# Performance work log

Hardware: AMD Instinct MI355X
Metric: run time of the kernel (lower is better)

The kernel has to match this reference:

```python
import jax, jax.numpy as jnp
import numpy as np

N = 8192
H = 512
E = 262144
NUM_LAYERS = 2
LAYER_DECAY = 0.4
INIT_W = 1e-05


def setup_inputs() -> dict:
    key = jax.random.key(0)
    ks = jax.random.split(key, 6)
    x = jax.random.normal(ks[0], (N, H), dtype=jnp.float32)
    rows = jax.random.randint(ks[1], (E,), 0, N, dtype=jnp.int32)
    cols = jax.random.randint(ks[2], (E,), 0, N, dtype=jnp.int32)
    vals = jax.random.uniform(ks[3], (E,), dtype=jnp.float32)
    # near-identity init as in GSS_GNNLayer (torch Linear: y = x @ W.T + b)
    W1 = jax.random.normal(ks[4], (H, H), dtype=jnp.float32) * INIT_W + jnp.eye(H, dtype=jnp.float32)
    b1 = jnp.zeros((H,), dtype=jnp.float32)
    W2 = jax.random.normal(ks[5], (H, H), dtype=jnp.float32) * INIT_W + jnp.eye(H, dtype=jnp.float32)
    b2 = jnp.zeros((H,), dtype=jnp.float32)
    return {"x": x, "rows": rows, "cols": cols, "vals": vals,
            "W1": W1, "b1": b1, "W2": W2, "b2": b2}


def _spmm(rows, cols, vals, dense):
    # sparse [N,N] @ dense [N,H] via gather + segment-sum scatter-add
    return jax.ops.segment_sum(vals[:, None] * dense[cols], rows, num_segments=N)


def _gcn_layer(x, rows, cols, vals, W1, b1, W2, b2):
    Ax = _spmm(rows, cols, vals, x)                      # [N,H]
    pre1 = Ax @ W1.T + b1
    Ax_x = _spmm(rows, cols, vals, Ax * x)               # A(Ax * x)
    pre2 = Ax_x @ W2.T + b2
    pre = pre1 + pre2
    return pre, jax.nn.elu(pre)


def reference(x, rows, cols, vals, W1, b1, W2, b2):
    residual = None
    for _ in range(NUM_LAYERS):  # shared weights across layers, as in source
        pre, x = _gcn_layer(x, rows, cols, vals, W1, b1, W2, b2)
        if residual is not None:
            x = residual + LAYER_DECAY * x
        residual = pre
    # decoder: row-wise L2 normalize (eps=1e-12 like F.normalize), dense gram, relu
    norm = jnp.maximum(jnp.linalg.norm(x, axis=1, keepdims=True), 1e-12)
    hidden_emb = x / norm
    adj_preds = jax.nn.relu(hidden_emb @ hidden_emb.T)   # [N,N]
    return adj_preds, hidden_emb
```

## Files before the change

kernel.cpp:

```cpp
#include <hip/hip_runtime.h>

#define N_NODES 8192
#define HDIM    512
#define NEDGE   262144

typedef __attribute__((ext_vector_type(8))) short bf16x8;
typedef __attribute__((ext_vector_type(4))) float f32x4;

__device__ inline unsigned short f2bf(float f) {
  unsigned u = __float_as_uint(f);
  unsigned r = (u + 0x7FFFu + ((u >> 16) & 1u)) >> 16;
  return (unsigned short)r;
}
__device__ inline float bf2f(short s) {
  return __uint_as_float(((unsigned)(unsigned short)s) << 16);
}

__device__ inline void gload16(const void* g, void* l) {
  __builtin_amdgcn_global_load_lds(
      (const __attribute__((address_space(1))) unsigned*)g,
      (__attribute__((address_space(3))) unsigned*)l, 16, 0, 0);
}

__device__ inline void wait_vmcnt_c(int n) {
  if (n == 8)      asm volatile("s_waitcnt vmcnt(8)" ::: "memory");
  else if (n == 4) asm volatile("s_waitcnt vmcnt(4)" ::: "memory");
  else if (n == 3) asm volatile("s_waitcnt vmcnt(3)" ::: "memory");
  else             asm volatile("s_waitcnt vmcnt(0)" ::: "memory");
}

__global__ __launch_bounds__(1024) void scan_kernel(const int* __restrict__ counts,
                                                    int* __restrict__ offs,
                                                    int* __restrict__ cursor) {
  __shared__ int s[1024];
  int tid = threadIdx.x;
  int local[8];
  int sum = 0;
#pragma unroll
  for (int i = 0; i < 8; ++i) { local[i] = counts[tid * 8 + i]; sum += local[i]; }
  s[tid] = sum;
  __syncthreads();
  for (int d = 1; d < 1024; d <<= 1) {
    int v = (tid >= d) ? s[tid - d] : 0;
    __syncthreads();
    s[tid] += v;
    __syncthreads();
  }
  int base = (tid > 0) ? s[tid - 1] : 0;
#pragma unroll
  for (int i = 0; i < 8; ++i) {
    offs[tid * 8 + i] = base;
    cursor[tid * 8 + i] = base;
    base += local[i];
  }
  if (tid == 1023) offs[8192] = base;
}

__global__ void scatter_kernel(const int* __restrict__ rows, const int* __restrict__ cols,
                               const float* __restrict__ vals, int* cursor,
                               int2* __restrict__ edges) {
  int e = blockIdx.x * 256 + threadIdx.x;
  int slot = atomicAdd(&cursor[rows[e]], 1);
  edges[slot] = make_int2(cols[e], __float_as_int(vals[e]));
}

template <int MODE>
__global__ __launch_bounds__(256) void spmm_bf(const int* __restrict__ offs,
                                               const int2* __restrict__ edges,
                                               const short* __restrict__ Xbf,
                                               const float* __restrict__ aux,
                                               short* __restrict__ outb,
                                               short* __restrict__ prodb) {
  int row = blockIdx.x * 4 + (threadIdx.x >> 6);
  int lane = threadIdx.x & 63;
  int h0 = lane * 8;
  float acc[8] = {0.f, 0.f, 0.f, 0.f, 0.f, 0.f, 0.f, 0.f};
  int e0 = offs[row], e1 = offs[row + 1];
  int p = e0;

  int2 ma0, ma1, ma2, ma3;
  bf16x8 xa0, xa1, xa2, xa3;

  if (p + 4 <= e1) {
    ma0 = edges[p]; ma1 = edges[p + 1]; ma2 = edges[p + 2]; ma3 = edges[p + 3];
    xa0 = *reinterpret_cast<const bf16x8*>(Xbf + (size_t)ma0.x * HDIM + h0);
    xa1 = *reinterpret_cast<const bf16x8*>(Xbf + (size_t)ma1.x * HDIM + h0);
    xa2 = *reinterpret_cast<const bf16x8*>(Xbf + (size_t)ma2.x * HDIM + h0);
    xa3 = *reinterpret_cast<const bf16x8*>(Xbf + (size_t)ma3.x * HDIM + h0);
    p += 4;
    for (; p + 4 <= e1; p += 4) {
      int2 mb0 = edges[p], mb1 = edges[p + 1], mb2 = edges[p + 2], mb3 = edges[p + 3];
      bf16x8 xb0 = *reinterpret_cast<const bf16x8*>(Xbf + (size_t)mb0.x * HDIM + h0);
      bf16x8 xb1 = *reinterpret_cast<const bf16x8*>(Xbf + (size_t)mb1.x * HDIM + h0);
      bf16x8 xb2 = *reinterpret_cast<const bf16x8*>(Xbf + (size_t)mb2.x * HDIM + h0);
      bf16x8 xb3 = *reinterpret_cast<const bf16x8*>(Xbf + (size_t)mb3.x * HDIM + h0);
      float v0 = __int_as_float(ma0.y), v1 = __int_as_float(ma1.y);
      float v2 = __int_as_float(ma2.y), v3 = __int_as_float(ma3.y);
#pragma unroll
      for (int j = 0; j < 8; ++j) {
        acc[j] = fmaf(v0, bf2f(xa0[j]), acc[j]);
        acc[j] = fmaf(v1, bf2f(xa1[j]), acc[j]);
        acc[j] = fmaf(v2, bf2f(xa2[j]), acc[j]);
        acc[j] = fmaf(v3, bf2f(xa3[j]), acc[j]);
      }
      ma0 = mb0; ma1 = mb1; ma2 = mb2; ma3 = mb3;
      xa0 = xb0; xa1 = xb1; xa2 = xb2; xa3 = xb3;
    }
    {
      float v0 = __int_as_float(ma0.y), v1 = __int_as_float(ma1.y);
      float v2 = __int_as_float(ma2.y), v3 = __int_as_float(ma3.y);
#pragma unroll
      for (int j = 0; j < 8; ++j) {
        acc[j] = fmaf(v0, bf2f(xa0[j]), acc[j]);
        acc[j] = fmaf(v1, bf2f(xa1[j]), acc[j]);
        acc[j] = fmaf(v2, bf2f(xa2[j]), acc[j]);
        acc[j] = fmaf(v3, bf2f(xa3[j]), acc[j]);
      }
    }
  }
  for (; p < e1; ++p) {
    int2 e = edges[p];
    float v = __int_as_float(e.y);
    bf16x8 xr = *reinterpret_cast<const bf16x8*>(Xbf + (size_t)e.x * HDIM + h0);
#pragma unroll
    for (int j = 0; j < 8; ++j) acc[j] = fmaf(v, bf2f(xr[j]), acc[j]);
  }

  bf16x8 o;
#pragma unroll
  for (int j = 0; j < 8; ++j) o[j] = (short)f2bf(acc[j]);
  *reinterpret_cast<bf16x8*>(outb + (size_t)row * 1024 + h0) = o;
  if (MODE != 2) {
    const float4* ap = reinterpret_cast<const float4*>(aux + (size_t)row * HDIM + h0);
    float4 a0 = ap[0], a1 = ap[1];
    float xv[8] = {a0.x, a0.y, a0.z, a0.w, a1.x, a1.y, a1.z, a1.w};
    if (MODE == 1) {
#pragma unroll
      for (int j = 0; j < 8; ++j) xv[j] = xv[j] > 0.f ? xv[j] : expm1f(xv[j]);
    }
    bf16x8 t;
#pragma unroll
    for (int j = 0; j < 8; ++j) t[j] = (short)f2bf(acc[j] * xv[j]);
    *reinterpret_cast<bf16x8*>(prodb + (size_t)row * HDIM + h0) = t;
  }
}

__device__ inline void cast8(const float* src, short* dst) {
  const float4* p = reinterpret_cast<const float4*>(src);
  float4 a = p[0], b = p[1];
  bf16x8 o;
  o[0] = (short)f2bf(a.x); o[1] = (short)f2bf(a.y);
  o[2] = (short)f2bf(a.z); o[3] = (short)f2bf(a.w);
  o[4] = (short)f2bf(b.x); o[5] = (short)f2bf(b.y);
  o[6] = (short)f2bf(b.z); o[7] = (short)f2bf(b.w);
  *reinterpret_cast<bf16x8*>(dst) = o;
}

__global__ void prep_kernel(const int* __restrict__ rows, int* __restrict__ counts,
                            const float* __restrict__ x,
                            const float* __restrict__ W1, const float* __restrict__ W2,
                            const float* __restrict__ b1, const float* __restrict__ b2,
                            short* __restrict__ Xbf, short* __restrict__ Bbuf,
                            float* __restrict__ b12) {
  int b = blockIdx.x;
  if (b < 1024) {
    int e = b * 256 + threadIdx.x;
    atomicAdd(&counts[rows[e]], 1);
  } else if (b < 3072) {
    int t = (b - 1024) * 256 + threadIdx.x;
    int row = t >> 6, c0 = (t & 63) * 8;
    cast8(x + (size_t)row * 512 + c0, Xbf + (size_t)row * 512 + c0);
  } else if (b < 3200) {
    int t = (b - 3072) * 256 + threadIdx.x;
    int row = t >> 6, c0 = (t & 63) * 8;
    cast8(W1 + (size_t)row * 512 + c0, Bbuf + (size_t)row * 1024 + c0);
  } else if (b < 3328) {
    int t = (b - 3200) * 256 + threadIdx.x;
    int row = t >> 6, c0 = (t & 63) * 8;
    cast8(W2 + (size_t)row * 512 + c0, Bbuf + (size_t)row * 1024 + 512 + c0);
  } else {
    int j = threadIdx.x;
    b12[j] = b1[j] + b2[j];
    b12[j + 256] = b1[j + 256] + b2[j + 256];
  }
}

__global__ __launch_bounds__(256) void rownorm_kernel(const float* __restrict__ X,
                                                      float* __restrict__ outf,
                                                      short* __restrict__ outb) {
  int row = blockIdx.x * 4 + (threadIdx.x >> 6);
  int lane = threadIdx.x & 63;
  int h0 = lane * 8;
  const float4* p = reinterpret_cast<const float4*>(X + (size_t)row * HDIM + h0);
  float4 a = p[0], b = p[1];
  float s = a.x * a.x + a.y * a.y + a.z * a.z + a.w * a.w +
            b.x * b.x + b.y * b.y + b.z * b.z + b.w * b.w;
#pragma unroll
  for (int off = 1; off < 64; off <<= 1) s += __shfl_xor(s, off, 64);
  float inv = 1.f / fmaxf(sqrtf(s), 1e-12f);
  a.x *= inv; a.y *= inv; a.z *= inv; a.w *= inv;
  b.x *= inv; b.y *= inv; b.z *= inv; b.w *= inv;
  float4* q = reinterpret_cast<float4*>(outf + (size_t)row * HDIM + h0);
  q[0] = a; q[1] = b;
  bf16x8 o;
  o[0] = (short)f2bf(a.x); o[1] = (short)f2bf(a.y);
  o[2] = (short)f2bf(a.z); o[3] = (short)f2bf(a.w);
  o[4] = (short)f2bf(b.x); o[5] = (short)f2bf(b.y);
  o[6] = (short)f2bf(b.z); o[7] = (short)f2bf(b.w);
  *reinterpret_cast<bf16x8*>(outb + (size_t)row * HDIM + h0) = o;
}

template <int MODE>
__global__ __launch_bounds__(256) void gemm_ring(const short* __restrict__ A,
                                                 const short* __restrict__ B,
                                                 int N, int K, int nbn,
                                                 const float* __restrict__ bias,
                                                 const float* __restrict__ resid,
                                                 float* __restrict__ out0,
                                                 short* __restrict__ out1bf) {
  __shared__ __align__(16) char lds[3 * 16384];
  int NK = K >> 5;

  int q = gridDim.x >> 3;
  int id = (blockIdx.x & 7) * q + (blockIdx.x >> 3);
  int bn = (id % nbn) * 128;
  int bm = (id / nbn) * 128;

  int tid = threadIdx.x;
  int wid = tid >> 6;
  int lane = tid & 63;
  int wm = wid >> 1, wn = wid & 1;
  int rlo = lane & 15;
  int khi = lane >> 4;
  int wbase = wid * 1024;

  size_t ldkB = (size_t)K * 2;
  const char* Ab = (const char*)A + (size_t)bm * ldkB;
  const char* Bb = (const char*)B + (size_t)bn * ldkB;
  int r4 = tid >> 2, c4 = tid & 3;

  f32x4 zero = {0.f, 0.f, 0.f, 0.f};
  f32x4 acc[4][4];
#pragma unroll
  for (int m = 0; m < 4; ++m)
#pragma unroll
    for (int n = 0; n < 4; ++n) acc[m][n] = zero;

  auto stage = [&](int s) {
    char* slot = lds + (s % 3) * 16384;
    size_t go = (size_t)s * 64 + c4 * 16;
    gload16(Ab + (size_t)r4 * ldkB + go,         slot + wbase);
    gload16(Ab + (size_t)(r4 + 64) * ldkB + go,  slot + 4096 + wbase);
    gload16(Bb + (size_t)r4 * ldkB + go,         slot + 8192 + wbase);
    gload16(Bb + (size_t)(r4 + 64) * ldkB + go,  slot + 12288 + wbase);
  };

  stage(0);
  stage(1);

  for (int s = 0; s < NK; ++s) {
    wait_vmcnt_c((s + 1 < NK) ? 4 : 0);
    __builtin_amdgcn_s_barrier();
    __builtin_amdgcn_sched_barrier(0);
    if (s + 2 < NK) stage(s + 2);

    const char* slot = lds + (s % 3) * 16384;
    bf16x8 av[4], bv[4];
#pragma unroll
    for (int m = 0; m < 4; ++m)
      av[m] = *reinterpret_cast<const bf16x8*>(
          slot + (wm * 64 + m * 16 + rlo) * 64 + khi * 16);
#pragma unroll
    for (int n = 0; n < 4; ++n)
      bv[n] = *reinterpret_cast<const bf16x8*>(
          slot + 8192 + (wn * 64 + n * 16 + rlo) * 64 + khi * 16);

    __builtin_amdgcn_s_setprio(1);
#pragma unroll
    for (int m = 0; m < 4; ++m)
#pragma unroll
      for (int n = 0; n < 4; ++n)
        acc[m][n] = __builtin_amdgcn_mfma_f32_16x16x32_bf16(av[m], bv[n], acc[m][n], 0, 0, 0);
    __builtin_amdgcn_s_setprio(0);
  }

  int obm = bm + wm * 64;
  int obn = bn + wn * 64;
  int crow = khi * 4;
#pragma unroll
  for (int n = 0; n < 4; ++n) {
    int c = obn + n * 16 + rlo;
    float bc = bias[c];
#pragma unroll
    for (int m = 0; m < 4; ++m) {
#pragma unroll
      for (int v = 0; v < 4; ++v) {
        int r = obm + m * 16 + crow + v;
        size_t idx = (size_t)r * N + c;
        float val = acc[m][n][v];
        if (MODE == 0) {
          float pvl = val + bc;
          out0[idx] = pvl;
          float e = pvl > 0.f ? pvl : expm1f(pvl);
          out1bf[idx] = (short)f2bf(e);
        } else {
          float pvl = val + bc;
          out0[idx] = resid[idx] + 0.4f * (pvl > 0.f ? pvl : expm1f(pvl));
        }
      }
    }
  }
}

__global__ __launch_bounds__(512, 4) void gram256(const short* __restrict__ H,
                                                  float* __restrict__ out) {
  __shared__ __align__(16) char lds[3 * 24576];
  const int NK = HDIM / 32;

  int id = (blockIdx.x & 7) * 256 + (blockIdx.x >> 3);
  int st = id >> 4, wt = id & 15;
  int bm = ((st >> 3) * 4 + (wt >> 2)) * 128;
  int bn = ((st & 7) * 4 + (wt & 3)) * 256;

  int tid = threadIdx.x;
  int wid = tid >> 6;
  int lane = tid & 63;
  int wr = wid >> 2;
  int wc = wid & 3;
  int rlo = lane & 15;
  int khi = lane >> 4;
  int wbase = wid * 1024;

  const char* Ab = (const char*)H + (size_t)bm * 1024;
  const char* Bb = (const char*)H + (size_t)bn * 1024;
  int r4 = tid >> 2, c4 = tid & 3;

  f32x4 zero = {0.f, 0.f, 0.f, 0.f};
  f32x4 acc[4][4];
#pragma unroll
  for (int m = 0; m < 4; ++m)
#pragma unroll
    for (int n = 0; n < 4; ++n) acc[m][n] = zero;

  auto stage = [&](int s) {
    char* slot = lds + (s % 3) * 24576;
    size_t go = (size_t)s * 64 + c4 * 16;
    gload16(Ab + (size_t)r4 * 1024 + go,         slot + wbase);
    gload16(Bb + (size_t)r4 * 1024 + go,         slot + 8192 + wbase);
    gload16(Bb + (size_t)(r4 + 128) * 1024 + go, slot + 16384 + wbase);
  };

  stage(0);
  stage(1);

  for (int s = 0; s < NK; ++s) {
    wait_vmcnt_c((s + 1 < NK) ? 3 : 0);
    __builtin_amdgcn_s_barrier();
    __builtin_amdgcn_sched_barrier(0);
    if (s + 2 < NK) stage(s + 2);

    const char* slot = lds + (s % 3) * 24576;
    bf16x8 av[4], bv[4];
#pragma unroll
    for (int m = 0; m < 4; ++m)
      av[m] = *reinterpret_cast<const bf16x8*>(
          slot + (wr * 64 + m * 16 + rlo) * 64 + khi * 16);
#pragma unroll
    for (int n = 0; n < 4; ++n)
      bv[n] = *reinterpret_cast<const bf16x8*>(
          slot + 8192 + (wc * 64 + n * 16 + rlo) * 64 + khi * 16);

    __builtin_amdgcn_s_setprio(1);
#pragma unroll
    for (int m = 0; m < 4; ++m)
#pragma unroll
      for (int n = 0; n < 4; ++n)
        acc[m][n] = __builtin_amdgcn_mfma_f32_16x16x32_bf16(av[m], bv[n], acc[m][n], 0, 0, 0);
    __builtin_amdgcn_s_setprio(0);
  }

  int obm = bm + wr * 64;
  int obn = bn + wc * 64;
  int crow = khi * 4;
#pragma unroll
  for (int m = 0; m < 4; ++m) {
#pragma unroll
    for (int n = 0; n < 4; ++n) {
      int c = obn + n * 16 + rlo;
#pragma unroll
      for (int v = 0; v < 4; ++v) {
        int r = obm + m * 16 + crow + v;
        float val = acc[m][n][v];
        out[(size_t)r * N_NODES + c] = val > 0.f ? val : 0.f;
      }
    }
  }
}

extern "C" void kernel_launch(void* const* d_in, const int* in_sizes, int n_in,
                              void* d_out, int out_size, void* d_ws, size_t ws_size,
                              hipStream_t stream) {
  const float* x  = (const float*)d_in[0];
  const int* rows = (const int*)d_in[1];
  const int* cols = (const int*)d_in[2];
  const float* vals = (const float*)d_in[3];
  const float* W1 = (const float*)d_in[4];
  const float* b1 = (const float*)d_in[5];
  const float* W2 = (const float*)d_in[6];
  const float* b2 = (const float*)d_in[7];

  float* out_adj = (float*)d_out;
  float* out_hid = out_adj + (size_t)N_NODES * N_NODES;

  char* w = (char*)d_ws;
  size_t off = 0;
  auto alloc = [&](size_t bytes) -> void* {
    void* p = w + off;
    off += (bytes + 255) & ~(size_t)255;
    return p;
  };
  int* counts   = (int*)alloc(8192 * sizeof(int));
  int* offs     = (int*)alloc(8193 * sizeof(int));
  int* cursor   = (int*)alloc(8192 * sizeof(int));
  int2* edges   = (int2*)alloc((size_t)NEDGE * sizeof(int2));
  float* b12    = (float*)alloc(HDIM * sizeof(float));
  short* Xbf    = (short*)alloc((size_t)N_NODES * HDIM * sizeof(short));
  short* Tbf    = (short*)alloc((size_t)N_NODES * HDIM * sizeof(short));
  short* Abuf   = (short*)alloc((size_t)N_NODES * 1024 * sizeof(short));
  short* Bbuf   = (short*)alloc((size_t)512 * 1024 * sizeof(short));
  float* pre1   = (float*)alloc((size_t)N_NODES * HDIM * sizeof(float));
  float* Hf     = (float*)alloc((size_t)N_NODES * HDIM * sizeof(float));
  short* Hbuf   = (short*)alloc((size_t)N_NODES * HDIM * sizeof(short));

  hipMemsetAsync(counts, 0, 8192 * sizeof(int), stream);
  prep_kernel<<<3329, 256, 0, stream>>>(rows, counts, x, W1, W2, b1, b2, Xbf, Bbuf, b12);
  scan_kernel<<<1, 1024, 0, stream>>>(counts, offs, cursor);
  scatter_kernel<<<NEDGE / 256, 256, 0, stream>>>(rows, cols, vals, cursor, edges);

  spmm_bf<0><<<2048, 256, 0, stream>>>(offs, edges, Xbf, x, Abuf, Tbf);
  spmm_bf<2><<<2048, 256, 0, stream>>>(offs, edges, Tbf, nullptr, Abuf + 512, nullptr);
  gemm_ring<0><<<256, 256, 0, stream>>>(Abuf, Bbuf, 512, 1024, 4, b12, nullptr, pre1, Xbf);

  spmm_bf<1><<<2048, 256, 0, stream>>>(offs, edges, Xbf, pre1, Abuf, Tbf);
  spmm_bf<2><<<2048, 256, 0, stream>>>(offs, edges, Tbf, nullptr, Abuf + 512, nullptr);
  gemm_ring<1><<<256, 256, 0, stream>>>(Abuf, Bbuf, 512, 1024, 4, b12, pre1, Hf, nullptr);

  rownorm_kernel<<<2048, 256, 0, stream>>>(Hf, out_hid, Hbuf);
  gram256<<<2048, 512, 0, stream>>>(Hbuf, out_adj);
}
```

Measured before the change: 315.7 us.

## Enlarge gram tile to 256x256 with 8-wave split-phase double-buffered pipeline

Replaces the 128x256 gram kernel with a 256x256 tile per block, so each wave computes a 128x64 output using 8x4 accumulators. The K loop now moves 128 elements per iteration, split into four quarter-loads across two double-buffered 64 KB LDS slots, with loads interleaved between MFMA phases. This halves the number of blocks and raises reuse of the operands fetched from global memory. In exchange it uses more registers, allows fewer resident blocks per CU, and needs a hand-scheduled waitcnt sequence. The gram kernel's output write of the 8192x8192 fp32 matrix is unchanged and probably dominates its cost.

```diff
diff --git a/kernel.cpp b/kernel.cpp
--- a/kernel.cpp
+++ b/kernel.cpp
@@ -24,6 +24,7 @@
 
 __device__ inline void wait_vmcnt_c(int n) {
   if (n == 8)      asm volatile("s_waitcnt vmcnt(8)" ::: "memory");
+  else if (n == 6) asm volatile("s_waitcnt vmcnt(6)" ::: "memory");
   else if (n == 4) asm volatile("s_waitcnt vmcnt(4)" ::: "memory");
   else if (n == 3) asm volatile("s_waitcnt vmcnt(3)" ::: "memory");
   else             asm volatile("s_waitcnt vmcnt(0)" ::: "memory");
@@ -312,14 +313,13 @@
   }
 }
 
-__global__ __launch_bounds__(512, 4) void gram256(const short* __restrict__ H,
-                                                  float* __restrict__ out) {
-  __shared__ __align__(16) char lds[3 * 24576];
-  const int NK = HDIM / 32;
-
-  int id = (blockIdx.x & 7) * 256 + (blockIdx.x >> 3);
+__global__ __launch_bounds__(512, 2) void gram8(const short* __restrict__ H,
+                                                float* __restrict__ out) {
+  __shared__ __align__(16) char lds[131072];
+
+  int id = (blockIdx.x & 7) * 128 + (blockIdx.x >> 3);
   int st = id >> 4, wt = id & 15;
-  int bm = ((st >> 3) * 4 + (wt >> 2)) * 128;
+  int bm = ((st >> 3) * 4 + (wt >> 2)) * 256;
   int bn = ((st & 7) * 4 + (wt & 3)) * 256;
 
   int tid = threadIdx.x;
@@ -336,54 +336,141 @@
   int r4 = tid >> 2, c4 = tid & 3;
 
   f32x4 zero = {0.f, 0.f, 0.f, 0.f};
-  f32x4 acc[4][4];
-#pragma unroll
-  for (int m = 0; m < 4; ++m)
+  f32x4 acc[8][4];
+#pragma unroll
+  for (int m = 0; m < 8; ++m)
 #pragma unroll
     for (int n = 0; n < 4; ++n) acc[m][n] = zero;
 
-  auto stage = [&](int s) {
-    char* slot = lds + (s % 3) * 24576;
-    size_t go = (size_t)s * 64 + c4 * 16;
-    gload16(Ab + (size_t)r4 * 1024 + go,         slot + wbase);
-    gload16(Bb + (size_t)r4 * 1024 + go,         slot + 8192 + wbase);
-    gload16(Bb + (size_t)(r4 + 128) * 1024 + go, slot + 16384 + wbase);
+  auto stage = [&](int kt, int p) {
+    char* buf = lds + ((kt & 1) << 16);
+    int off = (p == 0) ? 0 : (p == 1) ? 32768 : (p == 2) ? 16384 : 49152;
+    const char* src = (p == 0 || p == 2) ? Ab : Bb;
+    size_t go = (size_t)kt * 128 + ((p >> 1) ? 64 : 0) + c4 * 16;
+    gload16(src + (size_t)r4 * 1024 + go,         buf + off + wbase);
+    gload16(src + (size_t)(r4 + 128) * 1024 + go, buf + off + 8192 + wbase);
   };
 
-  stage(0);
-  stage(1);
-
-  for (int s = 0; s < NK; ++s) {
-    wait_vmcnt_c((s + 1 < NK) ? 3 : 0);
+  stage(0, 0); stage(0, 1); stage(0, 2); stage(0, 3);
+
+  bf16x8 av[4], bv[4];
+  const int arow = wr * 128 + rlo;
+  const int brow = wc * 64 + rlo;
+
+#pragma unroll 1
+  for (int kt = 0; kt < 7; ++kt) {
+    const char* buf = lds + ((kt & 1) << 16);
+    stage(kt + 1, 0);
+    wait_vmcnt_c(6);
     __builtin_amdgcn_s_barrier();
     __builtin_amdgcn_sched_barrier(0);
-    if (s + 2 < NK) stage(s + 2);
-
-    const char* slot = lds + (s % 3) * 24576;
-    bf16x8 av[4], bv[4];
-#pragma unroll
-    for (int m = 0; m < 4; ++m)
-      av[m] = *reinterpret_cast<const bf16x8*>(
-          slot + (wr * 64 + m * 16 + rlo) * 64 + khi * 16);
 #pragma unroll
     for (int n = 0; n < 4; ++n)
-      bv[n] = *reinterpret_cast<const bf16x8*>(
-          slot + 8192 + (wc * 64 + n * 16 + rlo) * 64 + khi * 16);
-
+      bv[n] = *reinterpret_cast<const bf16x8*>(buf + 32768 + (brow + n * 16) * 64 + khi * 16);
+#pragma unroll
+    for (int i = 0; i < 4; ++i)
+      av[i] = *reinterpret_cast<const bf16x8*>(buf + (arow + i * 16) * 64 + khi * 16);
     __builtin_amdgcn_s_setprio(1);
 #pragma unroll
-    for (int m = 0; m < 4; ++m)
-#pragma unroll
-      for (int n = 0; n < 4; ++n)
-        acc[m][n] = __builtin_amdgcn_mfma_f32_16x16x32_bf16(av[m], bv[n], acc[m][n], 0, 0, 0);
+    for (int i = 0; i < 4; ++i)
+#pragma unroll
+      for (int n = 0; n < 4; ++n)
+        acc[i][n] = __builtin_amdgcn_mfma_f32_16x16x32_bf16(av[i], bv[n], acc[i][n], 0, 0, 0);
     __builtin_amdgcn_s_setprio(0);
-  }
-
-  int obm = bm + wr * 64;
+    stage(kt + 1, 1);
+#pragma unroll
+    for (int i = 0; i < 4; ++i)
+      av[i] = *reinterpret_cast<const bf16x8*>(buf + (arow + 64 + i * 16) * 64 + khi * 16);
+    __builtin_amdgcn_s_setprio(1);
+#pragma unroll
+    for (int i = 0; i < 4; ++i)
+#pragma unroll
+      for (int n = 0; n < 4; ++n)
+        acc[4 + i][n] = __builtin_amdgcn_mfma_f32_16x16x32_bf16(av[i], bv[n], acc[4 + i][n], 0, 0, 0);
+    __builtin_amdgcn_s_setprio(0);
+    stage(kt + 1, 2);
+    wait_vmcnt_c(6);
+    __builtin_amdgcn_s_barrier();
+    __builtin_amdgcn_sched_barrier(0);
+#pragma unroll
+    for (int n = 0; n < 4; ++n)
+      bv[n] = *reinterpret_cast<const bf16x8*>(buf + 49152 + (brow + n * 16) * 64 + khi * 16);
+#pragma unroll
+    for (int i = 0; i < 4; ++i)
+      av[i] = *reinterpret_cast<const bf16x8*>(buf + 16384 + (arow + i * 16) * 64 + khi * 16);
+    __builtin_amdgcn_s_setprio(1);
+#pragma unroll
+    for (int i = 0; i < 4; ++i)
+#pragma unroll
+      for (int n = 0; n < 4; ++n)
+        acc[i][n] = __builtin_amdgcn_mfma_f32_16x16x32_bf16(av[i], bv[n], acc[i][n], 0, 0, 0);
+    __builtin_amdgcn_s_setprio(0);
+    stage(kt + 1, 3);
+#pragma unroll
+    for (int i = 0; i < 4; ++i)
+      av[i] = *reinterpret_cast<const bf16x8*>(buf + 16384 + (arow + 64 + i * 16) * 64 + khi * 16);
+    __builtin_amdgcn_s_setprio(1);
+#pragma unroll
+    for (int i = 0; i < 4; ++i)
+#pragma unroll
+      for (int n = 0; n < 4; ++n)
+        acc[4 + i][n] = __builtin_amdgcn_mfma_f32_16x16x32_bf16(av[i], bv[n], acc[4 + i][n], 0, 0, 0);
+    __builtin_amdgcn_s_setprio(0);
+  }
+
+  {
+    const char* buf = lds + ((7 & 1) << 16);
+    wait_vmcnt_c(4);
+    __builtin_amdgcn_s_barrier();
+    __builtin_amdgcn_sched_barrier(0);
+#pragma unroll
+    for (int n = 0; n < 4; ++n)
+      bv[n] = *reinterpret_cast<const bf16x8*>(buf + 32768 + (brow + n * 16) * 64 + khi * 16);
+#pragma unroll
+    for (int i = 0; i < 4; ++i)
+      av[i] = *reinterpret_cast<const bf16x8*>(buf + (arow + i * 16) * 64 + khi * 16);
+#pragma unroll
+    for (int i = 0; i < 4; ++i)
+#pragma unroll
+      for (int n = 0; n < 4; ++n)
+        acc[i][n] = __builtin_amdgcn_mfma_f32_16x16x32_bf16(av[i], bv[n], acc[i][n], 0, 0, 0);
+#pragma unroll
+    for (int i = 0; i < 4; ++i)
+      av[i] = *reinterpret_cast<const bf16x8*>(buf + (arow + 64 + i * 16) * 64 + khi * 16);
+#pragma unroll
+    for (int i = 0; i < 4; ++i)
+#pragma unroll
+      for (int n = 0; n < 4; ++n)
+        acc[4 + i][n] = __builtin_amdgcn_mfma_f32_16x16x32_bf16(av[i], bv[n], acc[4 + i][n], 0, 0, 0);
+    wait_vmcnt_c(0);
+    __builtin_amdgcn_s_barrier();
+    __builtin_amdgcn_sched_barrier(0);
+#pragma unroll
+    for (int n = 0; n < 4; ++n)
+      bv[n] = *reinterpret_cast<const bf16x8*>(buf + 49152 + (brow + n * 16) * 64 + khi * 16);
+#pragma unroll
+    for (int i = 0; i < 4; ++i)
+      av[i] = *reinterpret_cast<const bf16x8*>(buf + 16384 + (arow + i * 16) * 64 + khi * 16);
+#pragma unroll
+    for (int i = 0; i < 4; ++i)
+#pragma unroll
+      for (int n = 0; n < 4; ++n)
+        acc[i][n] = __builtin_amdgcn_mfma_f32_16x16x32_bf16(av[i], bv[n], acc[i][n], 0, 0, 0);
+#pragma unroll
+    for (int i = 0; i < 4; ++i)
+      av[i] = *reinterpret_cast<const bf16x8*>(buf + 16384 + (arow + 64 + i * 16) * 64 + khi * 16);
+#pragma unroll
+    for (int i = 0; i < 4; ++i)
+#pragma unroll
+      for (int n = 0; n < 4; ++n)
+        acc[4 + i][n] = __builtin_amdgcn_mfma_f32_16x16x32_bf16(av[i], bv[n], acc[4 + i][n], 0, 0, 0);
+  }
+
+  int obm = bm + wr * 128;
   int obn = bn + wc * 64;
   int crow = khi * 4;
 #pragma unroll
-  for (int m = 0; m < 4; ++m) {
+  for (int m = 0; m < 8; ++m) {
 #pragma unroll
     for (int n = 0; n < 4; ++n) {
       int c = obn + n * 16 + rlo;
@@ -446,5 +533,5 @@
   gemm_ring<1><<<256, 256, 0, stream>>>(Abuf, Bbuf, 512, 1024, 4, b12, pre1, Hf, nullptr);
 
   rownorm_kernel<<<2048, 256, 0, stream>>>(Hf, out_hid, Hbuf);
-  gram256<<<2048, 512, 0, stream>>>(Hbuf, out_adj);
-}
+  gram8<<<1024, 512, 0, stream>>>(Hbuf, out_adj);
+}
```

After: 334.9 us. 6.1% more time.

## Split SpMM into two column-half passes to shrink gather working set

Applied to the files above, without the earlier changes.

Each SpMM launch now handles only 256 of the 512 feature columns, with each lane loading 4 bf16 values instead of 8, and is launched twice with a column offset. The gathered source matrix slice per pass is half as large, which is meant to fit better in L2/MALL and improve the hit rate of the random row gathers. In exchange, the edge list is read twice and kernel launches double, and each gather becomes an 8-byte load instead of 16 bytes. The unused vmcnt(8) branch was also removed.

```diff
diff --git a/kernel.cpp b/kernel.cpp
--- a/kernel.cpp
+++ b/kernel.cpp
@@ -5,6 +5,7 @@
 #define NEDGE   262144
 
 typedef __attribute__((ext_vector_type(8))) short bf16x8;
+typedef __attribute__((ext_vector_type(4))) short bf16x4;
 typedef __attribute__((ext_vector_type(4))) float f32x4;
 
 __device__ inline unsigned short f2bf(float f) {
@@ -23,8 +24,7 @@
 }
 
 __device__ inline void wait_vmcnt_c(int n) {
-  if (n == 8)      asm volatile("s_waitcnt vmcnt(8)" ::: "memory");
-  else if (n == 4) asm volatile("s_waitcnt vmcnt(4)" ::: "memory");
+  if (n == 4)      asm volatile("s_waitcnt vmcnt(4)" ::: "memory");
   else if (n == 3) asm volatile("s_waitcnt vmcnt(3)" ::: "memory");
   else             asm volatile("s_waitcnt vmcnt(0)" ::: "memory");
 }
@@ -70,34 +70,35 @@
                                                const short* __restrict__ Xbf,
                                                const float* __restrict__ aux,
                                                short* __restrict__ outb,
-                                               short* __restrict__ prodb) {
+                                               short* __restrict__ prodb,
+                                               int coff) {
   int row = blockIdx.x * 4 + (threadIdx.x >> 6);
   int lane = threadIdx.x & 63;
-  int h0 = lane * 8;
-  float acc[8] = {0.f, 0.f, 0.f, 0.f, 0.f, 0.f, 0.f, 0.f};
+  int h0 = coff + lane * 4;
+  float acc[4] = {0.f, 0.f, 0.f, 0.f};
   int e0 = offs[row], e1 = offs[row + 1];
   int p = e0;
 
   int2 ma0, ma1, ma2, ma3;
-  bf16x8 xa0, xa1, xa2, xa3;
+  bf16x4 xa0, xa1, xa2, xa3;
 
   if (p + 4 <= e1) {
     ma0 = edges[p]; ma1 = edges[p + 1]; ma2 = edges[p + 2]; ma3 = edges[p + 3];
-    xa0 = *reinterpret_cast<const bf16x8*>(Xbf + (size_t)ma0.x * HDIM + h0);
-    xa1 = *reinterpret_cast<const bf16x8*>(Xbf + (size_t)ma1.x * HDIM + h0);
-    xa2 = *reinterpret_cast<const bf16x8*>(Xbf + (size_t)ma2.x * HDIM + h0);
-    xa3 = *reinterpret_cast<const bf16x8*>(Xbf + (size_t)ma3.x * HDIM + h0);
+    xa0 = *reinterpret_cast<const bf16x4*>(Xbf + (size_t)ma0.x * HDIM + h0);
+    xa1 = *reinterpret_cast<const bf16x4*>(Xbf + (size_t)ma1.x * HDIM + h0);
+    xa2 = *reinterpret_cast<const bf16x4*>(Xbf + (size_t)ma2.x * HDIM + h0);
+    xa3 = *reinterpret_cast<const bf16x4*>(Xbf + (size_t)ma3.x * HDIM + h0);
     p += 4;
     for (; p + 4 <= e1; p += 4) {
       int2 mb0 = edges[p], mb1 = edges[p + 1], mb2 = edges[p + 2], mb3 = edges[p + 3];
-      bf16x8 xb0 = *reinterpret_cast<const bf16x8*>(Xbf + (size_t)mb0.x * HDIM + h0);
-      bf16x8 xb1 = *reinterpret_cast<const bf16x8*>(Xbf + (size_t)mb1.x * HDIM + h0);
-      bf16x8 xb2 = *reinterpret_cast<const bf16x8*>(Xbf + (size_t)mb2.x * HDIM + h0);
-      bf16x8 xb3 = *reinterpret_cast<const bf16x8*>(Xbf + (size_t)mb3.x * HDIM + h0);
+      bf16x4 xb0 = *reinterpret_cast<const bf16x4*>(Xbf + (size_t)mb0.x * HDIM + h0);
+      bf16x4 xb1 = *reinterpret_cast<const bf16x4*>(Xbf + (size_t)mb1.x * HDIM + h0);
+      bf16x4 xb2 = *reinterpret_cast<const bf16x4*>(Xbf + (size_t)mb2.x * HDIM + h0);
+      bf16x4 xb3 = *reinterpret_cast<const bf16x4*>(Xbf + (size_t)mb3.x * HDIM + h0);
       float v0 = __int_as_float(ma0.y), v1 = __int_as_float(ma1.y);
       float v2 = __int_as_float(ma2.y), v3 = __int_as_float(ma3.y);
 #pragma unroll
-      for (int j = 0; j < 8; ++j) {
+      for (int j = 0; j < 4; ++j) {
         acc[j] = fmaf(v0, bf2f(xa0[j]), acc[j]);
         acc[j] = fmaf(v1, bf2f(xa1[j]), acc[j]);
         acc[j] = fmaf(v2, bf2f(xa2[j]), acc[j]);
@@ -110,7 +111,7 @@
       float v0 = __int_as_float(ma0.y), v1 = __int_as_float(ma1.y);
       float v2 = __int_as_float(ma2.y), v3 = __int_as_float(ma3.y);
 #pragma unroll
-      for (int j = 0; j < 8; ++j) {
+      for (int j = 0; j < 4; ++j) {
         acc[j] = fmaf(v0, bf2f(xa0[j]), acc[j]);
         acc[j] = fmaf(v1, bf2f(xa1[j]), acc[j]);
         acc[j] = fmaf(v2, bf2f(xa2[j]), acc[j]);
@@ -121,27 +122,26 @@
   for (; p < e1; ++p) {
     int2 e = edges[p];
     float v = __int_as_float(e.y);
-    bf16x8 xr = *reinterpret_cast<const bf16x8*>(Xbf + (size_t)e.x * HDIM + h0);
-#pragma unroll
-    for (int j = 0; j < 8; ++j) acc[j] = fmaf(v, bf2f(xr[j]), acc[j]);
-  }
-
-  bf16x8 o;
-#pragma unroll
-  for (int j = 0; j < 8; ++j) o[j] = (short)f2bf(acc[j]);
-  *reinterpret_cast<bf16x8*>(outb + (size_t)row * 1024 + h0) = o;
+    bf16x4 xr = *reinterpret_cast<const bf16x4*>(Xbf + (size_t)e.x * HDIM + h0);
+#pragma unroll
+    for (int j = 0; j < 4; ++j) acc[j] = fmaf(v, bf2f(xr[j]), acc[j]);
+  }
+
+  bf16x4 o;
+#pragma unroll
+  for (int j = 0; j < 4; ++j) o[j] = (short)f2bf(acc[j]);
+  *reinterpret_cast<bf16x4*>(outb + (size_t)row * 1024 + h0) = o;
   if (MODE != 2) {
-    const float4* ap = reinterpret_cast<const float4*>(aux + (size_t)row * HDIM + h0);
-    float4 a0 = ap[0], a1 = ap[1];
-    float xv[8] = {a0.x, a0.y, a0.z, a0.w, a1.x, a1.y, a1.z, a1.w};
+    float4 a0 = *reinterpret_cast<const float4*>(aux + (size_t)row * HDIM + h0);
+    float xv[4] = {a0.x, a0.y, a0.z, a0.w};
     if (MODE == 1) {
 #pragma unroll
-      for (int j = 0; j < 8; ++j) xv[j] = xv[j] > 0.f ? xv[j] : expm1f(xv[j]);
+      for (int j = 0; j < 4; ++j) xv[j] = xv[j] > 0.f ? xv[j] : expm1f(xv[j]);
     }
-    bf16x8 t;
-#pragma unroll
-    for (int j = 0; j < 8; ++j) t[j] = (short)f2bf(acc[j] * xv[j]);
-    *reinterpret_cast<bf16x8*>(prodb + (size_t)row * HDIM + h0) = t;
+    bf16x4 t;
+#pragma unroll
+    for (int j = 0; j < 4; ++j) t[j] = (short)f2bf(acc[j] * xv[j]);
+    *reinterpret_cast<bf16x4*>(prodb + (size_t)row * HDIM + h0) = t;
   }
 }
 
@@ -437,12 +437,16 @@
   scan_kernel<<<1, 1024, 0, stream>>>(counts, offs, cursor);
   scatter_kernel<<<NEDGE / 256, 256, 0, stream>>>(rows, cols, vals, cursor, edges);
 
-  spmm_bf<0><<<2048, 256, 0, stream>>>(offs, edges, Xbf, x, Abuf, Tbf);
-  spmm_bf<2><<<2048, 256, 0, stream>>>(offs, edges, Tbf, nullptr, Abuf + 512, nullptr);
+  spmm_bf<0><<<2048, 256, 0, stream>>>(offs, edges, Xbf, x, Abuf, Tbf, 0);
+  spmm_bf<0><<<2048, 256, 0, stream>>>(offs, edges, Xbf, x, Abuf, Tbf, 256);
+  spmm_bf<2><<<2048, 256, 0, stream>>>(offs, edges, Tbf, nullptr, Abuf + 512, nullptr, 0);
+  spmm_bf<2><<<2048, 256, 0, stream>>>(offs, edges, Tbf, nullptr, Abuf + 512, nullptr, 256);
   gemm_ring<0><<<256, 256, 0, stream>>>(Abuf, Bbuf, 512, 1024, 4, b12, nullptr, pre1, Xbf);
 
-  spmm_bf<1><<<2048, 256, 0, stream>>>(offs, edges, Xbf, pre1, Abuf, Tbf);
-  spmm_bf<2><<<2048, 256, 0, stream>>>(offs, edges, Tbf, nullptr, Abuf + 512, nullptr);
+  spmm_bf<1><<<2048, 256, 0, stream>>>(offs, edges, Xbf, pre1, Abuf, Tbf, 0);
+  spmm_bf<1><<<2048, 256, 0, stream>>>(offs, edges, Xbf, pre1, Abuf, Tbf, 256);
+  spmm_bf<2><<<2048, 256, 0, stream>>>(offs, edges, Tbf, nullptr, Abuf + 512, nullptr, 0);
+  spmm_bf<2><<<2048, 256, 0, stream>>>(offs, edges, Tbf, nullptr, Abuf + 512, nullptr, 256);
   gemm_ring<1><<<256, 256, 0, stream>>>(Abuf, Bbuf, 512, 1024, 4, b12, pre1, Hf, nullptr);
 
   rownorm_kernel<<<2048, 256, 0, stream>>>(Hf, out_hid, Hbuf);
```

Result: slower. 329.8 us (+4.5%).

## Enlarge gram tile to 256x256 with 4-slot LDS ring and phased MFMA pipeline

Applied to the files above, without the earlier changes.

Replaces the 128x256 gram kernel with a 256x256-tile version that uses 128KB of LDS as a 4-deep ring and occupancy 1. Each k-step is split into four phases that interleave global-to-LDS prefetch, LDS reads and MFMA blocks, with explicit vmcnt waits and barriers. The intent is more operand reuse per loaded byte and better overlap of loads with matrix math. In exchange it loses the latency hiding that multiple resident blocks gave, and it adds more barriers per step.

```diff
diff --git a/kernel.cpp b/kernel.cpp
--- a/kernel.cpp
+++ b/kernel.cpp
@@ -312,14 +312,13 @@
   }
 }
 
-__global__ __launch_bounds__(512, 4) void gram256(const short* __restrict__ H,
-                                                  float* __restrict__ out) {
-  __shared__ __align__(16) char lds[3 * 24576];
-  const int NK = HDIM / 32;
-
-  int id = (blockIdx.x & 7) * 256 + (blockIdx.x >> 3);
+__global__ __launch_bounds__(512, 1) void gram8p(const short* __restrict__ H,
+                                                 float* __restrict__ out) {
+  __shared__ __align__(16) char lds[131072];
+
+  int id = (blockIdx.x & 7) * 128 + (blockIdx.x >> 3);
   int st = id >> 4, wt = id & 15;
-  int bm = ((st >> 3) * 4 + (wt >> 2)) * 128;
+  int bm = ((st >> 3) * 4 + (wt >> 2)) * 256;
   int bn = ((st & 7) * 4 + (wt & 3)) * 256;
 
   int tid = threadIdx.x;
@@ -329,61 +328,83 @@
   int wc = wid & 3;
   int rlo = lane & 15;
   int khi = lane >> 4;
-  int wbase = wid * 1024;
-
-  const char* Ab = (const char*)H + (size_t)bm * 1024;
-  const char* Bb = (const char*)H + (size_t)bn * 1024;
+
+  const char* Hb = (const char*)H;
+  size_t abase = (size_t)bm * 1024;
+  size_t bbase = (size_t)bn * 1024;
   int r4 = tid >> 2, c4 = tid & 3;
 
+  auto call = [&](int u, int c) {
+    size_t base = (c < 2) ? abase : bbase;
+    int row0 = (c & 1) << 7;
+    const char* src = Hb + base + (size_t)(row0 + r4) * 1024 + (size_t)u * 64 + c4 * 16;
+    char* dst = lds + ((u & 3) << 15) + (c << 13) + tid * 16;
+    gload16(src, dst);
+  };
+
   f32x4 zero = {0.f, 0.f, 0.f, 0.f};
-  f32x4 acc[4][4];
-#pragma unroll
-  for (int m = 0; m < 4; ++m)
+  f32x4 acc[8][4];
+#pragma unroll
+  for (int m = 0; m < 8; ++m)
 #pragma unroll
     for (int n = 0; n < 4; ++n) acc[m][n] = zero;
 
-  auto stage = [&](int s) {
-    char* slot = lds + (s % 3) * 24576;
-    size_t go = (size_t)s * 64 + c4 * 16;
-    gload16(Ab + (size_t)r4 * 1024 + go,         slot + wbase);
-    gload16(Bb + (size_t)r4 * 1024 + go,         slot + 8192 + wbase);
-    gload16(Bb + (size_t)(r4 + 128) * 1024 + go, slot + 16384 + wbase);
-  };
-
-  stage(0);
-  stage(1);
-
-  for (int s = 0; s < NK; ++s) {
-    wait_vmcnt_c((s + 1 < NK) ? 3 : 0);
-    __builtin_amdgcn_s_barrier();
-    __builtin_amdgcn_sched_barrier(0);
-    if (s + 2 < NK) stage(s + 2);
-
-    const char* slot = lds + (s % 3) * 24576;
-    bf16x8 av[4], bv[4];
-#pragma unroll
-    for (int m = 0; m < 4; ++m)
-      av[m] = *reinterpret_cast<const bf16x8*>(
-          slot + (wr * 64 + m * 16 + rlo) * 64 + khi * 16);
-#pragma unroll
-    for (int n = 0; n < 4; ++n)
-      bv[n] = *reinterpret_cast<const bf16x8*>(
-          slot + 8192 + (wc * 64 + n * 16 + rlo) * 64 + khi * 16);
-
-    __builtin_amdgcn_s_setprio(1);
-#pragma unroll
-    for (int m = 0; m < 4; ++m)
-#pragma unroll
-      for (int n = 0; n < 4; ++n)
-        acc[m][n] = __builtin_amdgcn_mfma_f32_16x16x32_bf16(av[m], bv[n], acc[m][n], 0, 0, 0);
-    __builtin_amdgcn_s_setprio(0);
-  }
-
-  int obm = bm + wr * 64;
+#pragma unroll
+  for (int u = 0; u < 3; ++u)
+#pragma unroll
+    for (int c = 0; c < 4; ++c) call(u, c);
+  wait_vmcnt_c(8);
+  __builtin_amdgcn_s_barrier();
+  __builtin_amdgcn_sched_barrier(0);
+
+  bf16x8 av[4], bv[4];
+
+#pragma unroll 1
+  for (int s = 0; s < 8; ++s) {
+#pragma unroll
+    for (int p = 0; p < 4; ++p) {
+      int u = 2 * s + (p >> 1);
+      int w = 2 * s + 3 + (p >> 1);
+      int cb = (p & 1) * 2;
+      if (w < 16) { call(w, cb); call(w, cb + 1); }
+
+      const char* slot = lds + ((u & 3) << 15);
+      int h = p & 1;
+#pragma unroll
+      for (int i = 0; i < 4; ++i)
+        av[i] = *reinterpret_cast<const bf16x8*>(
+            slot + (wr << 13) + ((h * 4 + i) * 16 + rlo) * 64 + khi * 16);
+      if (h == 0) {
+#pragma unroll
+        for (int n = 0; n < 4; ++n)
+          bv[n] = *reinterpret_cast<const bf16x8*>(
+              slot + 16384 + ((wc >> 1) << 13) +
+              ((wc & 1) * 64 + n * 16 + rlo) * 64 + khi * 16);
+      }
+
+      if (p == 1) wait_vmcnt_c((s <= 6) ? 8 : 0);
+      if (p == 3) wait_vmcnt_c((s <= 5) ? 8 : (s == 6 ? 4 : 0));
+      __builtin_amdgcn_s_barrier();
+      __builtin_amdgcn_sched_barrier(0);
+
+      __builtin_amdgcn_s_setprio(1);
+#pragma unroll
+      for (int i = 0; i < 4; ++i)
+#pragma unroll
+        for (int n = 0; n < 4; ++n)
+          acc[h * 4 + i][n] =
+              __builtin_amdgcn_mfma_f32_16x16x32_bf16(av[i], bv[n], acc[h * 4 + i][n], 0, 0, 0);
+      __builtin_amdgcn_s_setprio(0);
+      __builtin_amdgcn_s_barrier();
+      __builtin_amdgcn_sched_barrier(0);
+    }
+  }
+
+  int obm = bm + wr * 128;
   int obn = bn + wc * 64;
   int crow = khi * 4;
 #pragma unroll
-  for (int m = 0; m < 4; ++m) {
+  for (int m = 0; m < 8; ++m) {
 #pragma unroll
     for (int n = 0; n < 4; ++n) {
       int c = obn + n * 16 + rlo;
@@ -446,5 +467,5 @@
   gemm_ring<1><<<256, 256, 0, stream>>>(Abuf, Bbuf, 512, 1024, 4, b12, pre1, Hf, nullptr);
 
   rownorm_kernel<<<2048, 256, 0, stream>>>(Hf, out_hid, Hbuf);
-  gram256<<<2048, 512, 0, stream>>>(Hbuf, out_adj);
-}
+  gram8p<<<1024, 512, 0, stream>>>(Hbuf, out_adj);
+}
```

Measured after the change: 344.0 us. 9.0% more time.
